# Performance work log

Measured on AMD Instinct MI355X. Metric: run time of the kernel, lower is better.

The kernel has to match this reference:

```python
import jax, jax.numpy as jnp
import numpy as np

SCALE = 4.0  # VeRA scale hyperparameter


def setup_inputs() -> dict:
    key = jax.random.key(0)
    ks = jax.random.split(key, 7)
    T, IN, OUT, R = 8192, 4096, 4096, 256
    return {
        "x": jax.random.normal(ks[0], (T, IN), dtype=jnp.float32),
        "base_weight": jax.random.normal(ks[1], (OUT, IN), dtype=jnp.float32) * 0.02,
        "base_bias": jax.random.normal(ks[2], (OUT,), dtype=jnp.float32) * 0.02,
        "vera_random_A": jax.random.normal(ks[3], (R, IN), dtype=jnp.float32) * (1.0 / np.sqrt(IN)),
        "vera_random_B": jax.random.normal(ks[4], (OUT, R), dtype=jnp.float32) * (1.0 / np.sqrt(R)),
        "vera_d": jax.random.normal(ks[5], (R,), dtype=jnp.float32) * 0.01,
        "vera_b": 0.1 * jnp.ones((OUT,), dtype=jnp.float32),
    }


def reference(x, base_weight, base_bias, vera_random_A, vera_random_B, vera_d, vera_b):
    # delta_W = scale * diag(vera_b) @ B @ diag(vera_d) @ A  -> row/col scaling, no diag matmuls
    # shapes: B (out, r), A (r, in), delta (out, in)
    delta = SCALE * jnp.einsum("or,ri->oi", vera_b[:, None] * vera_random_B, vera_d[:, None] * vera_random_A)
    # linear: y = x @ (W + delta)^T + bias
    return x @ (base_weight + delta).T + base_bias
```

## Files before the change

kernel.cpp:

```cpp
#include <hip/hip_runtime.h>


typedef __attribute__((ext_vector_type(8))) short short8;
typedef __attribute__((ext_vector_type(4))) float f32x4;

__device__ __forceinline__ unsigned short f2bf(float f) {
  union { float f; unsigned int u; } c; c.f = f;
  unsigned int u = c.u;
  unsigned int r = (u + 0x7fffu + ((u >> 16) & 1u)) >> 16;
  return (unsigned short)r;
}

__device__ __forceinline__ void gl2lds16(const unsigned short* g, unsigned short* l) {
  __builtin_amdgcn_global_load_lds(
      (const __attribute__((address_space(1))) unsigned int*)g,
      (__attribute__((address_space(3))) unsigned int*)l, 16, 0, 0);
}

__global__ __launch_bounds__(256) void k_cvt(const float* __restrict__ s,
                                             unsigned short* __restrict__ d, int n4) {
  int i = blockIdx.x * 256 + threadIdx.x;
  if (i >= n4) return;
  const float4 v = ((const float4*)s)[i];
  union { unsigned short u[4]; unsigned long long ll; } o;
  o.u[0] = f2bf(v.x); o.u[1] = f2bf(v.y); o.u[2] = f2bf(v.z); o.u[3] = f2bf(v.w);
  ((unsigned long long*)d)[i] = o.ll;
}

__global__ __launch_bounds__(256) void k_prep(const float* __restrict__ Bv,
                                              const float* __restrict__ Av,
                                              const float* __restrict__ dv,
                                              const float* __restrict__ bv,
                                              unsigned short* __restrict__ Bd,
                                              unsigned short* __restrict__ AbT) {
  int idx = blockIdx.x * 256 + threadIdx.x;
  int o = idx >> 8, r = idx & 255;
  Bd[idx]  = f2bf(4.0f * bv[o] * Bv[idx] * dv[r]);
  AbT[idx] = f2bf(Av[(size_t)r * 4096 + o]);
}

template <int FOLD>
__global__ __launch_bounds__(256) void gemm_bt(const unsigned short* __restrict__ Amat,
                                               const unsigned short* __restrict__ Bmat,
                                               int K, int N,
                                               const float* __restrict__ extra,
                                               float* __restrict__ outF,
                                               unsigned short* __restrict__ outB) {
  __shared__ unsigned short As[128 * 32];
  __shared__ unsigned short Bs[128 * 32];

  const int tid  = threadIdx.x;
  const int lane = tid & 63;
  const int wave = tid >> 6;
  const int wm   = wave >> 1;
  const int wn   = wave & 1;
  const int quad = lane >> 4;
  const int m16  = lane & 15;

  const int blockN = blockIdx.x * 128;
  const int blockM = blockIdx.y * 128;

  const int ldRow = lane >> 2;
  const int ldCol = (lane & 3) * 8;
  const int seg0  = wave * 2;

  const size_t aOff0 = (size_t)(blockM + seg0 * 16 + ldRow) * K + ldCol;
  const size_t aOff1 = (size_t)(blockM + seg0 * 16 + 16 + ldRow) * K + ldCol;
  const size_t bOff0 = (size_t)(blockN + seg0 * 16 + ldRow) * K + ldCol;
  const size_t bOff1 = (size_t)(blockN + seg0 * 16 + 16 + ldRow) * K + ldCol;

  unsigned short* lA0 = &As[(seg0 * 16 + ldRow) * 32 + ldCol];
  unsigned short* lA1 = &As[(seg0 * 16 + 16 + ldRow) * 32 + ldCol];
  unsigned short* lB0 = &Bs[(seg0 * 16 + ldRow) * 32 + ldCol];
  unsigned short* lB1 = &Bs[(seg0 * 16 + 16 + ldRow) * 32 + ldCol];

  f32x4 acc[4][4];
#pragma unroll
  for (int i = 0; i < 4; ++i)
#pragma unroll
    for (int j = 0; j < 4; ++j) acc[i][j] = (f32x4){0.f, 0.f, 0.f, 0.f};

  const short8* Asv = (const short8*)As;
  const short8* Bsv = (const short8*)Bs;

  for (int k0 = 0; k0 < K; k0 += 32) {
    __syncthreads();
    gl2lds16(Amat + aOff0 + k0, lA0);
    gl2lds16(Amat + aOff1 + k0, lA1);
    gl2lds16(Bmat + bOff0 + k0, lB0);
    gl2lds16(Bmat + bOff1 + k0, lB1);
    __syncthreads();

    short8 af[4], bf[4];
#pragma unroll
    for (int t = 0; t < 4; ++t) {
      af[t] = Asv[(wm * 64 + t * 16 + m16) * 4 + quad];
      bf[t] = Bsv[(wn * 64 + t * 16 + m16) * 4 + quad];
    }
#pragma unroll
    for (int mt = 0; mt < 4; ++mt)
#pragma unroll
      for (int nt = 0; nt < 4; ++nt)
        acc[mt][nt] = __builtin_amdgcn_mfma_f32_16x16x32_bf16(af[mt], bf[nt], acc[mt][nt], 0, 0, 0);
  }

#pragma unroll
  for (int mt = 0; mt < 4; ++mt) {
    const int row0 = blockM + wm * 64 + mt * 16 + quad * 4;
#pragma unroll
    for (int nt = 0; nt < 4; ++nt) {
      const int col = blockN + wn * 64 + nt * 16 + m16;
      f32x4 v = acc[mt][nt];
      if (FOLD) {
#pragma unroll
        for (int r = 0; r < 4; ++r) {
          size_t o = (size_t)(row0 + r) * N + col;
          outB[o] = f2bf(extra[o] + v[r]);
        }
      } else {
        const float bv = extra[col];
#pragma unroll
        for (int r = 0; r < 4; ++r) {
          size_t o = (size_t)(row0 + r) * N + col;
          outF[o] = v[r] + bv;
        }
      }
    }
  }
}

extern "C" void kernel_launch(void* const* d_in, const int* in_sizes, int n_in,
                              void* d_out, int out_size, void* d_ws, size_t ws_size,
                              hipStream_t stream) {
  const float* x    = (const float*)d_in[0];
  const float* W    = (const float*)d_in[1];
  const float* bias = (const float*)d_in[2];
  const float* A    = (const float*)d_in[3];
  const float* B    = (const float*)d_in[4];
  const float* dv   = (const float*)d_in[5];
  const float* bv   = (const float*)d_in[6];
  float* out = (float*)d_out;

  char* ws = (char*)d_ws;
  unsigned short* xb  = (unsigned short*)ws;
  unsigned short* Wc  = (unsigned short*)(ws + (size_t)(64 << 20));
  unsigned short* Bd  = (unsigned short*)(ws + (size_t)(96 << 20));
  unsigned short* AbT = (unsigned short*)(ws + (size_t)(98 << 20));

  hipLaunchKernelGGL(k_cvt, dim3(32768), dim3(256), 0, stream, x, xb, 8388608);
  hipLaunchKernelGGL(k_prep, dim3(4096), dim3(256), 0, stream, B, A, dv, bv, Bd, AbT);
  hipLaunchKernelGGL((gemm_bt<1>), dim3(32, 32), dim3(256), 0, stream,
                     Bd, AbT, 256, 4096, W, (float*)nullptr, Wc);
  hipLaunchKernelGGL((gemm_bt<0>), dim3(32, 64), dim3(256), 0, stream,
                     xb, Wc, 4096, 4096, bias, out, (unsigned short*)nullptr);
}
```

Before: 650.9 us.

## Swizzle LDS tiles in GEMM and fuse preprocessing kernels with tiled transpose

Applies an XOR swizzle to the global-to-LDS load columns and the matching fragment reads, so the MFMA operand loads from shared memory avoid bank conflicts. Merges the x conversion and the VeRA prep into one launch, and turns the strided A transpose into an LDS-tiled, coalesced transpose. This removes a launch and uncoalesced reads, at the cost of slightly more index arithmetic.

Result: no change. 640.1 us (-1.7%).

```diff
diff --git a/kernel.cpp b/kernel.cpp
--- a/kernel.cpp
+++ b/kernel.cpp
@@ -17,26 +17,45 @@
       (__attribute__((address_space(3))) unsigned int*)l, 16, 0, 0);
 }
 
-__global__ __launch_bounds__(256) void k_cvt(const float* __restrict__ s,
-                                             unsigned short* __restrict__ d, int n4) {
-  int i = blockIdx.x * 256 + threadIdx.x;
-  if (i >= n4) return;
-  const float4 v = ((const float4*)s)[i];
-  union { unsigned short u[4]; unsigned long long ll; } o;
-  o.u[0] = f2bf(v.x); o.u[1] = f2bf(v.y); o.u[2] = f2bf(v.z); o.u[3] = f2bf(v.w);
-  ((unsigned long long*)d)[i] = o.ll;
-}
-
-__global__ __launch_bounds__(256) void k_prep(const float* __restrict__ Bv,
-                                              const float* __restrict__ Av,
-                                              const float* __restrict__ dv,
-                                              const float* __restrict__ bv,
-                                              unsigned short* __restrict__ Bd,
-                                              unsigned short* __restrict__ AbT) {
-  int idx = blockIdx.x * 256 + threadIdx.x;
-  int o = idx >> 8, r = idx & 255;
-  Bd[idx]  = f2bf(4.0f * bv[o] * Bv[idx] * dv[r]);
-  AbT[idx] = f2bf(Av[(size_t)r * 4096 + o]);
+__global__ __launch_bounds__(256) void k_pre(const float* __restrict__ x,
+                                             unsigned short* __restrict__ xb,
+                                             const float* __restrict__ Bv,
+                                             const float* __restrict__ Av,
+                                             const float* __restrict__ dv,
+                                             const float* __restrict__ bv,
+                                             unsigned short* __restrict__ Bd,
+                                             unsigned short* __restrict__ AbT) {
+  __shared__ float tl[32][33];
+  const int blk = blockIdx.x;
+  const int tid = threadIdx.x;
+  if (blk < 32768) {
+    int i = blk * 256 + tid;
+    const float4 v = ((const float4*)x)[i];
+    union { unsigned short u[4]; unsigned long long ll; } o;
+    o.u[0] = f2bf(v.x); o.u[1] = f2bf(v.y); o.u[2] = f2bf(v.z); o.u[3] = f2bf(v.w);
+    ((unsigned long long*)xb)[i] = o.ll;
+  } else if (blk < 36864) {
+    int idx = (blk - 32768) * 256 + tid;
+    int o = idx >> 8, r = idx & 255;
+    Bd[idx] = f2bf(4.0f * bv[o] * Bv[idx] * dv[r]);
+  } else {
+    int blk2 = blk - 36864;
+    int ti = blk2 >> 3;
+    int tr = blk2 & 7;
+#pragma unroll
+    for (int s = 0; s < 4; ++s) {
+      int r = tr * 32 + s * 8 + (tid >> 5);
+      int i = ti * 32 + (tid & 31);
+      tl[s * 8 + (tid >> 5)][tid & 31] = Av[(size_t)r * 4096 + i];
+    }
+    __syncthreads();
+#pragma unroll
+    for (int s = 0; s < 4; ++s) {
+      int iloc = s * 8 + (tid >> 5);
+      int rloc = tid & 31;
+      AbT[(size_t)(ti * 32 + iloc) * 256 + tr * 32 + rloc] = f2bf(tl[rloc][iloc]);
+    }
+  }
 }
 
 template <int FOLD>
@@ -60,19 +79,20 @@
   const int blockN = blockIdx.x * 128;
   const int blockM = blockIdx.y * 128;
 
-  const int ldRow = lane >> 2;
-  const int ldCol = (lane & 3) * 8;
-  const int seg0  = wave * 2;
+  const int ldRow  = lane >> 2;
+  const int dstCol = (lane & 3) * 8;
+  const int srcCol = ((lane & 3) ^ ((lane >> 4) & 3)) * 8;
+  const int seg0   = wave * 2;
 
-  const size_t aOff0 = (size_t)(blockM + seg0 * 16 + ldRow) * K + ldCol;
-  const size_t aOff1 = (size_t)(blockM + seg0 * 16 + 16 + ldRow) * K + ldCol;
-  const size_t bOff0 = (size_t)(blockN + seg0 * 16 + ldRow) * K + ldCol;
-  const size_t bOff1 = (size_t)(blockN + seg0 * 16 + 16 + ldRow) * K + ldCol;
+  const size_t aOff0 = (size_t)(blockM + seg0 * 16 + ldRow) * K + srcCol;
+  const size_t aOff1 = (size_t)(blockM + seg0 * 16 + 16 + ldRow) * K + srcCol;
+  const size_t bOff0 = (size_t)(blockN + seg0 * 16 + ldRow) * K + srcCol;
+  const size_t bOff1 = (size_t)(blockN + seg0 * 16 + 16 + ldRow) * K + srcCol;
 
-  unsigned short* lA0 = &As[(seg0 * 16 + ldRow) * 32 + ldCol];
-  unsigned short* lA1 = &As[(seg0 * 16 + 16 + ldRow) * 32 + ldCol];
-  unsigned short* lB0 = &Bs[(seg0 * 16 + ldRow) * 32 + ldCol];
-  unsigned short* lB1 = &Bs[(seg0 * 16 + 16 + ldRow) * 32 + ldCol];
+  unsigned short* lA0 = &As[(seg0 * 16 + ldRow) * 32 + dstCol];
+  unsigned short* lA1 = &As[(seg0 * 16 + 16 + ldRow) * 32 + dstCol];
+  unsigned short* lB0 = &Bs[(seg0 * 16 + ldRow) * 32 + dstCol];
+  unsigned short* lB1 = &Bs[(seg0 * 16 + 16 + ldRow) * 32 + dstCol];
 
   f32x4 acc[4][4];
 #pragma unroll
@@ -82,6 +102,7 @@
 
   const short8* Asv = (const short8*)As;
   const short8* Bsv = (const short8*)Bs;
+  const int qsw = quad ^ ((m16 >> 2) & 3);
 
   for (int k0 = 0; k0 < K; k0 += 32) {
     __syncthreads();
@@ -94,8 +115,8 @@
     short8 af[4], bf[4];
 #pragma unroll
     for (int t = 0; t < 4; ++t) {
-      af[t] = Asv[(wm * 64 + t * 16 + m16) * 4 + quad];
-      bf[t] = Bsv[(wn * 64 + t * 16 + m16) * 4 + quad];
+      af[t] = Asv[(wm * 64 + t * 16 + m16) * 4 + qsw];
+      bf[t] = Bsv[(wn * 64 + t * 16 + m16) * 4 + qsw];
     }
 #pragma unroll
     for (int mt = 0; mt < 4; ++mt)
@@ -147,8 +168,8 @@
   unsigned short* Bd  = (unsigned short*)(ws + (size_t)(96 << 20));
   unsigned short* AbT = (unsigned short*)(ws + (size_t)(98 << 20));
 
-  hipLaunchKernelGGL(k_cvt, dim3(32768), dim3(256), 0, stream, x, xb, 8388608);
-  hipLaunchKernelGGL(k_prep, dim3(4096), dim3(256), 0, stream, B, A, dv, bv, Bd, AbT);
+  hipLaunchKernelGGL(k_pre, dim3(37888), dim3(256), 0, stream,
+                     x, xb, B, A, dv, bv, Bd, AbT);
   hipLaunchKernelGGL((gemm_bt<1>), dim3(32, 32), dim3(256), 0, stream,
                      Bd, AbT, 256, 4096, W, (float*)nullptr, Wc);
   hipLaunchKernelGGL((gemm_bt<0>), dim3(32, 64), dim3(256), 0, stream,
```
